# Performance work log

Hardware: AMD Instinct MI355X
Metric: run time of the kernel (lower is better)

## Reference

```python
import jax, jax.numpy as jnp
import numpy as np

B, C, H, W, S = 32, 512, 32, 32, 4
HW = H * W
OUT = HW // S  # conv1/conv2 out channels = 256
EPS = 1e-5


def setup_inputs() -> dict:
    key = jax.random.key(0)
    ks = jax.random.split(key, 8)
    d = {}
    d["x"] = jax.random.normal(ks[0], (B, C, H, W), jnp.float32)
    # conv1 / bn1 (operate on x_flat with 'channels' = h*w)
    d["w1"] = jax.random.normal(ks[1], (OUT, HW), jnp.float32) * 0.02
    d["b1"] = jnp.zeros((OUT,), jnp.float32)
    d["g1"] = jnp.ones((OUT,), jnp.float32)
    d["be1"] = jnp.zeros((OUT,), jnp.float32)
    d["m1"] = jax.random.normal(ks[2], (OUT,), jnp.float32) * 0.01
    d["v1"] = jnp.ones((OUT,), jnp.float32)
    # conv2 / bn2
    d["w2"] = jax.random.normal(ks[3], (OUT, HW), jnp.float32) * 0.02
    d["b2"] = jnp.zeros((OUT,), jnp.float32)
    d["g2"] = jnp.ones((OUT,), jnp.float32)
    d["be2"] = jnp.zeros((OUT,), jnp.float32)
    d["m2"] = jax.random.normal(ks[4], (OUT,), jnp.float32) * 0.01
    d["v2"] = jnp.ones((OUT,), jnp.float32)
    # conv3 / bn3 (1x1 conv on the real channel dim c)
    d["w3"] = jax.random.normal(ks[5], (C, C), jnp.float32) * 0.02
    d["b3"] = jnp.zeros((C,), jnp.float32)
    d["g3"] = jnp.ones((C,), jnp.float32)
    d["be3"] = jnp.zeros((C,), jnp.float32)
    d["m3"] = jax.random.normal(ks[6], (C,), jnp.float32) * 0.01
    d["v3"] = jnp.ones((C,), jnp.float32)
    # conv4: 1x1 conv mapping 1+2c channels -> 1
    d["w4"] = jax.random.normal(ks[7], (1 + 2 * C,), jnp.float32) * 0.02
    d["b4"] = jnp.zeros((), jnp.float32)
    return d


def _bn1d(t, g, be, m, v):
    # t: [b, o, c]; BatchNorm (eval mode) over channel axis 1
    scale = g / jnp.sqrt(v + EPS)
    return (t - m[:, None]) * scale[:, None] + be[:, None]


def reference(x, w1, b1, g1, be1, m1, v1,
              w2, b2, g2, be2, m2, v2,
              w3, b3, g3, be3, m3, v3,
              w4, b4):
    b, c, h, w = x.shape
    # x_flat: [b, h*w, c] -- conv1/conv2 are 1x1 convs over 'channels' = h*w
    xf = x.reshape(b, c, h * w).transpose(0, 2, 1)
    theta = jax.nn.relu(_bn1d(jnp.einsum('oq,bqc->boc', w1, xf) + b1[:, None],
                              g1, be1, m1, v1))  # [b, OUT, c]
    phi = jax.nn.relu(_bn1d(jnp.einsum('oq,bqc->boc', w2, xf) + b2[:, None],
                            g2, be2, m2, v2))    # [b, OUT, c]
    # per-batch conv2d-as-matmul loop collapses to one batched GEMM:
    # affinity[b, i, j] = sum_k phi[b, k, i] * theta[b, k, j]
    aff = jnp.einsum('bki,bkj->bij', phi, theta)  # [b, c, c]
    # x_embed: 1x1 conv + BN + ReLU + global average pool -> [b, c]
    scale3 = g3 / jnp.sqrt(v3 + EPS)
    xe = jnp.einsum('oc,bchw->bohw', w3, x) + b3[:, None, None]
    xe = jax.nn.relu((xe - m3[:, None, None]) * scale3[:, None, None]
                     + be3[:, None, None])
    xe = xe.mean(axis=(2, 3))  # [b, c]
    # conv4 over y = cat([x_embed, affinity_a, affinity_b], dim=1):
    # affinity_a[b,i,0,p] = aff[b,i,p]; affinity_b[b,i,0,p] = aff[b,p,i]
    logits = (w4[0] * xe
              + jnp.einsum('i,bip->bp', w4[1:1 + c], aff)
              + jnp.einsum('i,bpi->bp', w4[1 + c:], aff)
              + b4)
    a = jax.nn.sigmoid(logits)  # [b, c]
    return x * a[:, :, None, None]
```

## Files before the change

kernel.cpp:

```cpp
#include <hip/hip_runtime.h>
#include <math.h>

#define BB   32
#define CC   512
#define HWW  1024
#define OUTC 256
#define EPSV 1e-5f

typedef __attribute__((ext_vector_type(8))) short bfrag;
typedef __attribute__((ext_vector_type(4))) float f32x4;
typedef __attribute__((ext_vector_type(4))) unsigned int u32x4;

__device__ inline unsigned short f2bf(float x){
  unsigned int uu = __float_as_uint(x);
  uu += 0x7fff + ((uu >> 16) & 1);
  return (unsigned short)(uu >> 16);
}
__device__ inline float bf2f(unsigned short h){
  return __uint_as_float(((unsigned int)h) << 16);
}
__device__ inline void packpair(float v0, float v1, unsigned int& hw, unsigned int& lw){
  unsigned short h0 = f2bf(v0), h1 = f2bf(v1);
  unsigned short l0 = f2bf(v0 - bf2f(h0)), l1 = f2bf(v1 - bf2f(h1));
  hw = (unsigned int)h0 | ((unsigned int)h1 << 16);
  lw = (unsigned int)l0 | ((unsigned int)l1 << 16);
}


__global__ __launch_bounds__(256) void prep(
    const float* __restrict__ x,
    const float* __restrict__ w1, const float* __restrict__ w2,
    const float* __restrict__ w3,
    unsigned short* __restrict__ Xhi, unsigned short* __restrict__ Xlo,
    unsigned short* __restrict__ XThi,
    unsigned short* __restrict__ Whi, unsigned short* __restrict__ Wlo,
    unsigned short* __restrict__ W3hi,
    float* __restrict__ accz)
{
  const int tid = threadIdx.x;
  if (blockIdx.z == 32) {
    int worker = (blockIdx.y * 16 + blockIdx.x) * 256 + tid;
    accz[worker] = 0.f;
#pragma unroll
    for (int s = 0; s < 2; ++s) {
      int cid  = worker * 2 + s;
      int tile = cid >> 6, l = cid & 63;
      int o = (tile >> 5) * 16 + (l & 15);
      int k = (tile & 31) * 32 + (l >> 4) * 8;
      const float* src = (o < 256) ? (w1 + (size_t)o * 1024 + k)
                                   : (w2 + (size_t)(o - 256) * 1024 + k);
      u32x4 hv, lv;
#pragma unroll
      for (int j = 0; j < 4; ++j) {
        unsigned int hw, lw;
        packpair(src[2 * j], src[2 * j + 1], hw, lw);
        hv[j] = hw; lv[j] = lw;
      }
      size_t base = (size_t)tile * 512 + (size_t)l * 8;
      *(u32x4*)(Whi + base) = hv;
      *(u32x4*)(Wlo + base) = lv;
    }
    {
      int tile = worker >> 6, l = worker & 63;
      int o = (tile >> 4) * 16 + (l & 15);
      int c = (tile & 15) * 32 + (l >> 4) * 8;
      const float* src = w3 + (size_t)o * 512 + c;
      u32x4 hv;
#pragma unroll
      for (int j = 0; j < 4; ++j) {
        unsigned short h0 = f2bf(src[2 * j]), h1 = f2bf(src[2 * j + 1]);
        hv[j] = (unsigned int)h0 | ((unsigned int)h1 << 16);
      }
      *(u32x4*)(W3hi + (size_t)tile * 512 + (size_t)l * 8) = hv;
    }
    return;
  }
  __shared__ float T[64][65];
  const int b = blockIdx.z, c0 = blockIdx.y * 64, p0 = blockIdx.x * 64;
  const int tr = tid >> 4, tc4 = (tid & 15) * 4;
  const float* xb = x + (size_t)b * 524288;
#pragma unroll
  for (int r = 0; r < 4; ++r) {
    int cl = tr + r * 16;
    float4 v = *(const float4*)(xb + (size_t)(c0 + cl) * 1024 + p0 + tc4);
    T[cl][tc4 + 0] = v.x; T[cl][tc4 + 1] = v.y;
    T[cl][tc4 + 2] = v.z; T[cl][tc4 + 3] = v.w;
  }
  __syncthreads();
#pragma unroll
  for (int s = 0; s < 2; ++s) {
    int cid  = tid + s * 256;
    int tile = cid >> 6, l = cid & 63;
    int tileC = tile >> 1, tileP = tile & 1;
    int cl = tileC * 16 + (l & 15);
    int pl = tileP * 32 + (l >> 4) * 8;
    u32x4 hv, lv;
#pragma unroll
    for (int j = 0; j < 4; ++j) {
      unsigned int hw, lw;
      packpair(T[cl][pl + 2 * j], T[cl][pl + 2 * j + 1], hw, lw);
      hv[j] = hw; lv[j] = lw;
    }
    size_t base = (size_t)b * 524288
                + ((size_t)((c0 + cl) >> 4) * 32 + (size_t)((p0 + pl) >> 5)) * 512
                + (size_t)l * 8;
    *(u32x4*)(Xhi + base) = hv;
    *(u32x4*)(Xlo + base) = lv;
  }
#pragma unroll
  for (int s = 0; s < 2; ++s) {
    int cid  = tid + s * 256;
    int tile = cid >> 6, l = cid & 63;
    int tileP = tile >> 1, tileC = tile & 1;
    int pl = tileP * 16 + (l & 15);
    int cl = tileC * 32 + (l >> 4) * 8;
    u32x4 hv;
#pragma unroll
    for (int j = 0; j < 4; ++j) {
      unsigned short h0 = f2bf(T[cl + 2 * j][pl]);
      unsigned short h1 = f2bf(T[cl + 2 * j + 1][pl]);
      hv[j] = (unsigned int)h0 | ((unsigned int)h1 << 16);
    }
    size_t base = (size_t)b * 524288
                + ((size_t)((p0 + pl) >> 4) * 16 + (size_t)((c0 + cl) >> 5)) * 512
                + (size_t)l * 8;
    *(u32x4*)(XThi + base) = hv;
  }
}

__global__ __launch_bounds__(256, 3) void gemm_fused(
    const unsigned short* __restrict__ Xhi, const unsigned short* __restrict__ Xlo,
    const unsigned short* __restrict__ Whi, const unsigned short* __restrict__ Wlo,
    const unsigned short* __restrict__ W3hi, const unsigned short* __restrict__ XThi,
    const float* __restrict__ b1p, const float* __restrict__ g1p,
    const float* __restrict__ be1p, const float* __restrict__ m1p, const float* __restrict__ v1p,
    const float* __restrict__ b2p, const float* __restrict__ g2p,
    const float* __restrict__ be2p, const float* __restrict__ m2p, const float* __restrict__ v2p,
    const float* __restrict__ b3p, const float* __restrict__ g3p,
    const float* __restrict__ be3p, const float* __restrict__ m3p, const float* __restrict__ v3p,
    const float* __restrict__ w4,
    float* __restrict__ P2, float* __restrict__ u, float* __restrict__ t,
    float* __restrict__ xe_acc)
{
  const int fid  = blockIdx.x;
  const int tid  = threadIdx.x;
  const int wave = tid >> 6, lane = tid & 63;
  const int fr = lane & 15, fq = lane >> 4;

  if (fid < 512) {
    const int xcd = fid & 7;
    const int n0  = ((fid >> 3) & 3) * 128;
    const int bc  = ((fid >> 5) << 3) | xcd;
    const int b   = bc >> 2;
    const int c0  = (bc & 3) * 128;
    const int wm = wave & 1, wn = wave >> 1;

    const bfrag* Ah = (const bfrag*)Xhi + (size_t)b * 65536
                    + (size_t)((c0 >> 4) + wm * 4) * 2048 + lane;
    const bfrag* Al = (const bfrag*)Xlo + (size_t)b * 65536
                    + (size_t)((c0 >> 4) + wm * 4) * 2048 + lane;
    const bfrag* Bh = (const bfrag*)Whi + (size_t)((n0 >> 4) + wn * 4) * 2048 + lane;
    const bfrag* Bl = (const bfrag*)Wlo + (size_t)((n0 >> 4) + wn * 4) * 2048 + lane;

    f32x4 acc[4][4];
    const f32x4 zz = {0.f, 0.f, 0.f, 0.f};
#pragma unroll
    for (int i = 0; i < 4; ++i)
#pragma unroll
      for (int j = 0; j < 4; ++j) acc[i][j] = zz;

#pragma unroll 2
    for (int kq = 0; kq < 32; ++kq) {
      bfrag ah[4], al[4], bh[4], bl[4];
#pragma unroll
      for (int j = 0; j < 4; ++j) {
        bh[j] = Bh[(size_t)j * 2048 + kq * 64];
        bl[j] = Bl[(size_t)j * 2048 + kq * 64];
      }
#pragma unroll
      for (int i = 0; i < 4; ++i) {
        ah[i] = Ah[(size_t)i * 2048 + kq * 64];
        al[i] = Al[(size_t)i * 2048 + kq * 64];
      }
#pragma unroll
      for (int i = 0; i < 4; ++i)
#pragma unroll
        for (int j = 0; j < 4; ++j) {
          acc[i][j] = __builtin_amdgcn_mfma_f32_16x16x32_bf16(ah[i], bh[j], acc[i][j], 0, 0, 0);
          acc[i][j] = __builtin_amdgcn_mfma_f32_16x16x32_bf16(ah[i], bl[j], acc[i][j], 0, 0, 0);
          acc[i][j] = __builtin_amdgcn_mfma_f32_16x16x32_bf16(al[i], bh[j], acc[i][j], 0, 0, 0);
        }
    }

    const float *bias, *gg, *bes, *mm, *vv_; int cof;
    if (n0 < 256) { bias = b1p; gg = g1p; bes = be1p; mm = m1p; vv_ = v1p; cof = 0; }
    else          { bias = b2p; gg = g2p; bes = be2p; mm = m2p; vv_ = v2p; cof = 256; }
    const float* wsel = (n0 < 256) ? (w4 + 513) : (w4 + 1);
    float* dsel = (n0 < 256) ? (t + b * 256) : (u + b * 256);
    const int cobase = (n0 - cof) + wn * 64;
    float wt[4][4];
#pragma unroll
    for (int i = 0; i < 4; ++i)
#pragma unroll
      for (int r = 0; r < 4; ++r)
        wt[i][r] = wsel[c0 + wm * 64 + i * 16 + fq * 4 + r];

#pragma unroll
    for (int j = 0; j < 4; ++j) {
      int co = n0 + wn * 64 + j * 16 + fr;
      int q = co - cof;
      float s  = gg[q] * rsqrtf(vv_[q] + EPSV);
      float sh = (bias[q] - mm[q]) * s + bes[q];
      float psum = 0.f;
#pragma unroll
      for (int i = 0; i < 4; ++i) {
        int crow = c0 + wm * 64 + i * 16 + fq * 4;
        float* dst = P2 + ((size_t)b * 512 + crow) * 512 + co;
#pragma unroll
        for (int r = 0; r < 4; ++r) {
          float val = fmaxf(acc[i][j][r] * s + sh, 0.f);
          dst[(size_t)r * 512] = val;
          psum += wt[i][r] * val;
        }
      }
      psum += __shfl_xor(psum, 16);
      psum += __shfl_xor(psum, 32);
      if (fq == 0) atomicAdd(&dsel[cobase + j * 16 + fr], psum);
    }
  } else {
    const int h  = fid - 512;
    const int n0 = (h & 7) * 128;
    const int m0 = ((h >> 3) & 3) * 128;
    const int b  = h >> 5;
    const int wm = wave & 1, wn = wave >> 1;

    const bfrag* Af = (const bfrag*)W3hi + (size_t)((m0 >> 4) + wm * 4) * 1024 + lane;
    const bfrag* Bf = (const bfrag*)XThi + (size_t)b * 65536
                    + (size_t)((n0 >> 4) + wn * 4) * 1024 + lane;

    f32x4 acc[4][4];
    const f32x4 zz = {0.f, 0.f, 0.f, 0.f};
#pragma unroll
    for (int i = 0; i < 4; ++i)
#pragma unroll
      for (int j = 0; j < 4; ++j) acc[i][j] = zz;

#pragma unroll 2
    for (int kq = 0; kq < 16; ++kq) {
      bfrag af[4], bf4[4];
#pragma unroll
      for (int i = 0; i < 4; ++i)
        af[i] = Af[(size_t)i * 1024 + kq * 64];
#pragma unroll
      for (int j = 0; j < 4; ++j)
        bf4[j] = Bf[(size_t)j * 1024 + kq * 64];
#pragma unroll
      for (int i = 0; i < 4; ++i)
#pragma unroll
        for (int j = 0; j < 4; ++j)
          acc[i][j] = __builtin_amdgcn_mfma_f32_16x16x32_bf16(af[i], bf4[j], acc[i][j], 0, 0, 0);
    }

#pragma unroll
    for (int i = 0; i < 4; ++i) {
#pragma unroll
      for (int r = 0; r < 4; ++r) {
        int o = m0 + wm * 64 + i * 16 + fq * 4 + r;
        float s  = g3p[o] * rsqrtf(v3p[o] + EPSV);
        float sh = (b3p[o] - m3p[o]) * s + be3p[o];
        float v = fmaxf(acc[i][0][r] * s + sh, 0.f) + fmaxf(acc[i][1][r] * s + sh, 0.f)
                + fmaxf(acc[i][2][r] * s + sh, 0.f) + fmaxf(acc[i][3][r] * s + sh, 0.f);
        v += __shfl_xor(v, 1); v += __shfl_xor(v, 2);
        v += __shfl_xor(v, 4); v += __shfl_xor(v, 8);
        if (fr == 0) atomicAdd(&xe_acc[b * 512 + o], v);
      }
    }
  }
}

__global__ __launch_bounds__(256) void k4_gate_out(
    const float* __restrict__ P2, const float* __restrict__ u,
    const float* __restrict__ t, const float* __restrict__ xe_acc,
    const float* __restrict__ w4, const float* __restrict__ b4,
    const float* __restrict__ x, float* __restrict__ out)
{
  __shared__ float us[256], ts[256];
  const int b = blockIdx.x;
  us[threadIdx.x] = u[b * 256 + threadIdx.x];
  ts[threadIdx.x] = t[b * 256 + threadIdx.x];
  __syncthreads();
  const int wave = threadIdx.x >> 6, lane = threadIdx.x & 63;
  const int p = blockIdx.y * 4 + wave;
  const float* row = P2 + ((size_t)b * 512 + p) * 512;
  float4 th = *(const float4*)&row[lane * 4];
  float4 ph = *(const float4*)&row[256 + lane * 4];
  int ki = lane * 4;
  float rs = th.x * us[ki] + th.y * us[ki + 1] + th.z * us[ki + 2] + th.w * us[ki + 3]
           + ph.x * ts[ki] + ph.y * ts[ki + 1] + ph.z * ts[ki + 2] + ph.w * ts[ki + 3];
  rs += __shfl_xor(rs, 1);  rs += __shfl_xor(rs, 2);  rs += __shfl_xor(rs, 4);
  rs += __shfl_xor(rs, 8);  rs += __shfl_xor(rs, 16); rs += __shfl_xor(rs, 32);
  float xe = xe_acc[b * 512 + p] * (1.f / 1024.f);
  float logit = w4[0] * xe + rs + b4[0];
  float a = 1.f / (1.f + expf(-logit));
  const float4* xr = (const float4*)(x + ((size_t)b * 512 + p) * 1024);
  float4* orow = (float4*)(out + ((size_t)b * 512 + p) * 1024);
#pragma unroll
  for (int r2 = 0; r2 < 4; ++r2) {
    float4 xv = xr[lane + r2 * 64];
    float4 ov; ov.x = xv.x * a; ov.y = xv.y * a; ov.z = xv.z * a; ov.w = xv.w * a;
    orow[lane + r2 * 64] = ov;
  }
}

__global__ __launch_bounds__(256) void k1_theta_phi(
    const float* __restrict__ x,
    const float* __restrict__ w1, const float* __restrict__ b1,
    const float* __restrict__ g1, const float* __restrict__ be1,
    const float* __restrict__ m1, const float* __restrict__ v1,
    const float* __restrict__ w2, const float* __restrict__ b2,
    const float* __restrict__ g2, const float* __restrict__ be2,
    const float* __restrict__ m2, const float* __restrict__ v2,
    float* __restrict__ P)
{
  __shared__ __align__(16) float Ws[32][68];
  __shared__ __align__(16) float Xs[32][68];
  const int b  = blockIdx.z;
  const int o0 = blockIdx.y * 64;
  const int c0 = blockIdx.x * 64;
  const int tid = threadIdx.x;
  const int tx = tid & 15, ty = tid >> 4;
  const float* __restrict__ Wbase = (o0 < OUTC) ? (w1 + (size_t)o0 * HWW)
                                                : (w2 + (size_t)(o0 - OUTC) * HWW);
  const float* __restrict__ xb = x + (size_t)b * CC * HWW;
  float acc[4][4] = {{0.f}};
  for (int k0 = 0; k0 < HWW; k0 += 32) {
#pragma unroll
    for (int r = 0; r < 2; ++r) {
      int id  = tid + (r << 8);
      int row = id >> 3;
      int cg  = (id & 7) << 2;
      float4 wv = *(const float4*)(Wbase + (size_t)row * HWW + k0 + cg);
      Ws[cg+0][row] = wv.x; Ws[cg+1][row] = wv.y; Ws[cg+2][row] = wv.z; Ws[cg+3][row] = wv.w;
      float4 xv = *(const float4*)(xb + (size_t)(c0 + row) * HWW + k0 + cg);
      Xs[cg+0][row] = xv.x; Xs[cg+1][row] = xv.y; Xs[cg+2][row] = xv.z; Xs[cg+3][row] = xv.w;
    }
    __syncthreads();
#pragma unroll
    for (int k = 0; k < 32; ++k) {
      float4 av = *(const float4*)&Ws[k][ty * 4];
      float4 bv = *(const float4*)&Xs[k][tx * 4];
      acc[0][0] += av.x*bv.x; acc[0][1] += av.x*bv.y; acc[0][2] += av.x*bv.z; acc[0][3] += av.x*bv.w;
      acc[1][0] += av.y*bv.x; acc[1][1] += av.y*bv.y; acc[1][2] += av.y*bv.z; acc[1][3] += av.y*bv.w;
      acc[2][0] += av.z*bv.x; acc[2][1] += av.z*bv.y; acc[2][2] += av.z*bv.z; acc[2][3] += av.z*bv.w;
      acc[3][0] += av.w*bv.x; acc[3][1] += av.w*bv.y; acc[3][2] += av.w*bv.z; acc[3][3] += av.w*bv.w;
    }
    __syncthreads();
  }
  const float *bias, *g, *be, *m, *v; int ob;
  if (o0 < OUTC) { bias = b1; g = g1; be = be1; m = m1; v = v1; ob = o0; }
  else           { bias = b2; g = g2; be = be2; m = m2; v = v2; ob = o0 - OUTC; }
#pragma unroll
  for (int i = 0; i < 4; ++i) {
    int oi = ob + ty * 4 + i;
    float sc = g[oi] * rsqrtf(v[oi] + EPSV);
    float sh = be[oi] - m[oi] * sc;
    float bb = bias[oi];
    float4 ov;
    ov.x = fmaxf((acc[i][0] + bb) * sc + sh, 0.f);
    ov.y = fmaxf((acc[i][1] + bb) * sc + sh, 0.f);
    ov.z = fmaxf((acc[i][2] + bb) * sc + sh, 0.f);
    ov.w = fmaxf((acc[i][3] + bb) * sc + sh, 0.f);
    int oo = o0 + ty * 4 + i;
    *(float4*)(P + ((size_t)b * 512 + oo) * 512 + c0 + tx * 4) = ov;
  }
}

__global__ __launch_bounds__(256) void k2_xe(
    const float* __restrict__ x, const float* __restrict__ w3,
    const float* __restrict__ b3, const float* __restrict__ g3,
    const float* __restrict__ be3, const float* __restrict__ m3,
    const float* __restrict__ v3, float* __restrict__ xe_acc)
{
  __shared__ __align__(16) float As[32][68];
  __shared__ __align__(16) float Bs[32][68];
  const int b  = blockIdx.z;
  const int o0 = blockIdx.y * 64;
  const int p0 = blockIdx.x * 64;
  const int tid = threadIdx.x;
  const int tx = tid & 15, ty = tid >> 4;
  const float* __restrict__ xb = x + (size_t)b * CC * HWW;
  float acc[4][4] = {{0.f}};
  for (int ck = 0; ck < CC; ck += 32) {
#pragma unroll
    for (int r = 0; r < 2; ++r) {
      int id  = tid + (r << 8);
      int row = id >> 3;
      int cg  = (id & 7) << 2;
      float4 wv = *(const float4*)(w3 + (size_t)(o0 + row) * CC + ck + cg);
      As[cg+0][row] = wv.x; As[cg+1][row] = wv.y; As[cg+2][row] = wv.z; As[cg+3][row] = wv.w;
      int brow = id >> 4;
      int pg   = (id & 15) << 2;
      float4 xv = *(const float4*)(xb + (size_t)(ck + brow) * HWW + p0 + pg);
      *(float4*)&Bs[brow][pg] = xv;
    }
    __syncthreads();
#pragma unroll
    for (int k = 0; k < 32; ++k) {
      float4 av = *(const float4*)&As[k][ty * 4];
      float4 bv = *(const float4*)&Bs[k][tx * 4];
      acc[0][0] += av.x*bv.x; acc[0][1] += av.x*bv.y; acc[0][2] += av.x*bv.z; acc[0][3] += av.x*bv.w;
      acc[1][0] += av.y*bv.x; acc[1][1] += av.y*bv.y; acc[1][2] += av.y*bv.z; acc[1][3] += av.y*bv.w;
      acc[2][0] += av.z*bv.x; acc[2][1] += av.z*bv.y; acc[2][2] += av.z*bv.z; acc[2][3] += av.z*bv.w;
      acc[3][0] += av.w*bv.x; acc[3][1] += av.w*bv.y; acc[3][2] += av.w*bv.z; acc[3][3] += av.w*bv.w;
    }
    __syncthreads();
  }
#pragma unroll
  for (int i = 0; i < 4; ++i) {
    int oo = o0 + ty * 4 + i;
    float sc = g3[oo] * rsqrtf(v3[oo] + EPSV);
    float sh = be3[oo] - m3[oo] * sc;
    float bb = b3[oo];
    float ps = fmaxf((acc[i][0] + bb) * sc + sh, 0.f)
             + fmaxf((acc[i][1] + bb) * sc + sh, 0.f)
             + fmaxf((acc[i][2] + bb) * sc + sh, 0.f)
             + fmaxf((acc[i][3] + bb) * sc + sh, 0.f);
    ps += __shfl_xor(ps, 1);
    ps += __shfl_xor(ps, 2);
    ps += __shfl_xor(ps, 4);
    ps += __shfl_xor(ps, 8);
    if (tx == 0) atomicAdd(&xe_acc[b * CC + oo], ps);
  }
}

__global__ __launch_bounds__(256) void k3_ut(
    const float* __restrict__ P, const float* __restrict__ w4,
    float* __restrict__ u, float* __restrict__ t)
{
  const int b = blockIdx.x;
  const int wv = threadIdx.x >> 6, lane = threadIdx.x & 63;
  const int k = blockIdx.y * 4 + wv;
  const float* __restrict__ w4a = w4 + 1;
  const float* __restrict__ w4b = w4 + 1 + CC;
  const float* __restrict__ throw_ = P + ((size_t)b * 512 + k) * 512;
  const float* __restrict__ phrow  = P + ((size_t)b * 512 + 256 + k) * 512;
  float su = 0.f, st = 0.f;
#pragma unroll
  for (int i = lane; i < CC; i += 64) {
    su += w4a[i] * phrow[i];
    st += w4b[i] * throw_[i];
  }
#pragma unroll
  for (int off = 32; off > 0; off >>= 1) {
    su += __shfl_down(su, off);
    st += __shfl_down(st, off);
  }
  if (lane == 0) { u[b * OUTC + k] = su; t[b * OUTC + k] = st; }
}

__global__ __launch_bounds__(256) void k4_gate(
    const float* __restrict__ P, const float* __restrict__ u,
    const float* __restrict__ t, const float* __restrict__ xe_acc,
    const float* __restrict__ w4, const float* __restrict__ b4,
    float* __restrict__ amul)
{
  __shared__ float us[256], ts[256];
  const int b = blockIdx.x;
  const int p = blockIdx.y * 256 + threadIdx.x;
  us[threadIdx.x] = u[b * OUTC + threadIdx.x];
  ts[threadIdx.x] = t[b * OUTC + threadIdx.x];
  __syncthreads();
  const float* __restrict__ theta = P + (size_t)b * 512 * 512;
  const float* __restrict__ phi   = theta + 256 * 512;
  float r = 0.f, s = 0.f;
#pragma unroll 8
  for (int k = 0; k < OUTC; ++k) {
    r += us[k] * theta[(size_t)k * 512 + p];
    s += ts[k] * phi[(size_t)k * 512 + p];
  }
  float xe = xe_acc[b * CC + p] * (1.0f / 1024.0f);
  float logit = w4[0] * xe + r + s + b4[0];
  amul[b * CC + p] = 1.0f / (1.0f + expf(-logit));
}

__global__ __launch_bounds__(256) void k5_out(
    const float* __restrict__ x, const float* __restrict__ amul,
    float* __restrict__ out)
{
  int i = blockIdx.x * 256 + threadIdx.x;
  float4 xv = ((const float4*)x)[i];
  float a = amul[i >> 8];
  float4 ov; ov.x = xv.x * a; ov.y = xv.y * a; ov.z = xv.z * a; ov.w = xv.w * a;
  ((float4*)out)[i] = ov;
}

extern "C" void kernel_launch(void* const* d_in, const int* in_sizes, int n_in,
                              void* d_out, int out_size, void* d_ws, size_t ws_size,
                              hipStream_t stream)
{
  (void)in_sizes; (void)n_in; (void)out_size;
  const float* x   = (const float*)d_in[0];
  const float* w1  = (const float*)d_in[1];
  const float* b1  = (const float*)d_in[2];
  const float* g1  = (const float*)d_in[3];
  const float* be1 = (const float*)d_in[4];
  const float* m1  = (const float*)d_in[5];
  const float* v1  = (const float*)d_in[6];
  const float* w2  = (const float*)d_in[7];
  const float* b2  = (const float*)d_in[8];
  const float* g2  = (const float*)d_in[9];
  const float* be2 = (const float*)d_in[10];
  const float* m2  = (const float*)d_in[11];
  const float* v2  = (const float*)d_in[12];
  const float* w3  = (const float*)d_in[13];
  const float* b3  = (const float*)d_in[14];
  const float* g3  = (const float*)d_in[15];
  const float* be3 = (const float*)d_in[16];
  const float* m3  = (const float*)d_in[17];
  const float* v3  = (const float*)d_in[18];
  const float* w4  = (const float*)d_in[19];
  const float* b4  = (const float*)d_in[20];
  float* out = (float*)d_out;

  if (ws_size >= 136970240ull) {
    float* P2     = (float*)d_ws;
    float* xe_acc = P2 + 8388608;
    float* u      = P2 + 8404992;
    float* t      = P2 + 8413184;
    unsigned short* Xhi  = (unsigned short*)((char*)d_ws + 33685504);
    unsigned short* Xlo  = Xhi + 16777216;
    unsigned short* XThi = Xlo + 16777216;
    unsigned short* Whi  = XThi + 16777216;
    unsigned short* Wlo  = Whi + 524288;
    unsigned short* W3hi = Wlo + 524288;

    prep<<<dim3(16, 8, 33), 256, 0, stream>>>(x, w1, w2, w3, Xhi, Xlo, XThi,
                                              Whi, Wlo, W3hi, xe_acc);
    gemm_fused<<<dim3(1536), 256, 0, stream>>>(Xhi, Xlo, Whi, Wlo, W3hi, XThi,
        b1, g1, be1, m1, v1, b2, g2, be2, m2, v2, b3, g3, be3, m3, v3,
        w4, P2, u, t, xe_acc);
    k4_gate_out<<<dim3(32, 128), 256, 0, stream>>>(P2, u, t, xe_acc, w4, b4, x, out);
  } else {
    float* P      = (float*)d_ws;
    float* xe_acc = P + (size_t)BB * 512 * 512;
    float* u      = xe_acc + BB * CC;
    float* t      = u + BB * OUTC;
    float* amul   = t + BB * OUTC;

    hipMemsetAsync(xe_acc, 0, (size_t)BB * CC * sizeof(float), stream);

    dim3 blk(256);
    k1_theta_phi<<<dim3(8, 8, BB), blk, 0, stream>>>(x, w1, b1, g1, be1, m1, v1,
                                                     w2, b2, g2, be2, m2, v2, P);
    k2_xe<<<dim3(16, 8, BB), blk, 0, stream>>>(x, w3, b3, g3, be3, m3, v3, xe_acc);
    k3_ut<<<dim3(BB, 64), blk, 0, stream>>>(P, w4, u, t);
    k4_gate<<<dim3(BB, 2), blk, 0, stream>>>(P, u, t, xe_acc, w4, b4, amul);
    k5_out<<<dim3((BB * CC * HWW / 4) / 256), blk, 0, stream>>>(x, amul, out);
  }
}
```

Measured before the change: 269.2 us.

## Stage GEMM operands through double-buffered LDS with async global-to-LDS loads

Both GEMM paths in the fused kernel now stage their A/B fragments through a 64 KB shared-memory double buffer. Each wave issues global_load_lds copies for its own operand slice, and all waves then read the tiles from LDS. Previously every wave loaded its fragments straight from global memory, so the two waves sharing a row or column tile loaded the same data twice. The change removes that duplicate traffic and overlaps the next k-step's loads with the current MFMAs. In exchange it adds two block barriers per iteration and lowers the occupancy hint from 3 to 2 blocks per CU because of the LDS footprint.

New measurement: 257.4 us. 4.4% less time.

```diff
diff --git a/kernel.cpp b/kernel.cpp
--- a/kernel.cpp
+++ b/kernel.cpp
@@ -25,6 +25,11 @@
   hw = (unsigned int)h0 | ((unsigned int)h1 << 16);
   lw = (unsigned int)l0 | ((unsigned int)l1 << 16);
 }
+
+#define ASYNC16(g, l) \
+  __builtin_amdgcn_global_load_lds((const __attribute__((address_space(1))) unsigned int*)(g), \
+                                   (__attribute__((address_space(3))) unsigned int*)(l), 16, 0, 0)
+#define WAITV(N) asm volatile("s_waitcnt vmcnt(" #N ")" ::: "memory")
 
 
 __global__ __launch_bounds__(256) void prep(
@@ -128,7 +133,7 @@
   }
 }
 
-__global__ __launch_bounds__(256, 3) void gemm_fused(
+__global__ __launch_bounds__(256, 2) void gemm_fused(
     const unsigned short* __restrict__ Xhi, const unsigned short* __restrict__ Xlo,
     const unsigned short* __restrict__ Whi, const unsigned short* __restrict__ Wlo,
     const unsigned short* __restrict__ W3hi, const unsigned short* __restrict__ XThi,
@@ -142,6 +147,7 @@
     float* __restrict__ P2, float* __restrict__ u, float* __restrict__ t,
     float* __restrict__ xe_acc)
 {
+  __shared__ unsigned short smem[32768];
   const int fid  = blockIdx.x;
   const int tid  = threadIdx.x;
   const int wave = tid >> 6, lane = tid & 63;
@@ -155,12 +161,13 @@
     const int c0  = (bc & 3) * 128;
     const int wm = wave & 1, wn = wave >> 1;
 
-    const bfrag* Ah = (const bfrag*)Xhi + (size_t)b * 65536
-                    + (size_t)((c0 >> 4) + wm * 4) * 2048 + lane;
-    const bfrag* Al = (const bfrag*)Xlo + (size_t)b * 65536
-                    + (size_t)((c0 >> 4) + wm * 4) * 2048 + lane;
-    const bfrag* Bh = (const bfrag*)Whi + (size_t)((n0 >> 4) + wn * 4) * 2048 + lane;
-    const bfrag* Bl = (const bfrag*)Wlo + (size_t)((n0 >> 4) + wn * 4) * 2048 + lane;
+    const unsigned short* gsrc;
+    int ldst;
+    if (wave == 0)      { gsrc = Xhi + (size_t)b * 524288 + (size_t)(c0 >> 4) * 16384; ldst = 0; }
+    else if (wave == 1) { gsrc = Xlo + (size_t)b * 524288 + (size_t)(c0 >> 4) * 16384; ldst = 4096; }
+    else if (wave == 2) { gsrc = Whi + (size_t)(n0 >> 4) * 16384; ldst = 8192; }
+    else                { gsrc = Wlo + (size_t)(n0 >> 4) * 16384; ldst = 12288; }
+    gsrc += (size_t)lane * 8;
 
     f32x4 acc[4][4];
     const f32x4 zz = {0.f, 0.f, 0.f, 0.f};
@@ -169,18 +176,36 @@
 #pragma unroll
       for (int j = 0; j < 4; ++j) acc[i][j] = zz;
 
-#pragma unroll 2
+#pragma unroll
+    for (int i = 0; i < 8; ++i)
+      ASYNC16(gsrc + (size_t)i * 16384, smem + ldst + i * 512);
+
+    int cur = 0;
     for (int kq = 0; kq < 32; ++kq) {
+      __builtin_amdgcn_sched_barrier(0);
+      if (kq + 1 < 32) {
+        unsigned short* nb = smem + (cur ^ 1) * 16384 + ldst;
+#pragma unroll
+        for (int i = 0; i < 8; ++i)
+          ASYNC16(gsrc + (size_t)i * 16384 + (kq + 1) * 512, nb + i * 512);
+        WAITV(8);
+      } else {
+        WAITV(0);
+      }
+      __builtin_amdgcn_s_barrier();
+      __builtin_amdgcn_sched_barrier(0);
+
+      const unsigned short* bufc = smem + cur * 16384;
       bfrag ah[4], al[4], bh[4], bl[4];
 #pragma unroll
+      for (int i = 0; i < 4; ++i) {
+        ah[i] = *(const bfrag*)&bufc[(wm * 4 + i) * 512 + lane * 8];
+        al[i] = *(const bfrag*)&bufc[4096 + (wm * 4 + i) * 512 + lane * 8];
+      }
+#pragma unroll
       for (int j = 0; j < 4; ++j) {
-        bh[j] = Bh[(size_t)j * 2048 + kq * 64];
-        bl[j] = Bl[(size_t)j * 2048 + kq * 64];
-      }
-#pragma unroll
-      for (int i = 0; i < 4; ++i) {
-        ah[i] = Ah[(size_t)i * 2048 + kq * 64];
-        al[i] = Al[(size_t)i * 2048 + kq * 64];
+        bh[j] = *(const bfrag*)&bufc[8192 + (wn * 4 + j) * 512 + lane * 8];
+        bl[j] = *(const bfrag*)&bufc[12288 + (wn * 4 + j) * 512 + lane * 8];
       }
 #pragma unroll
       for (int i = 0; i < 4; ++i)
@@ -190,7 +215,11 @@
           acc[i][j] = __builtin_amdgcn_mfma_f32_16x16x32_bf16(ah[i], bl[j], acc[i][j], 0, 0, 0);
           acc[i][j] = __builtin_amdgcn_mfma_f32_16x16x32_bf16(al[i], bh[j], acc[i][j], 0, 0, 0);
         }
-    }
+      __builtin_amdgcn_sched_barrier(0);
+      __builtin_amdgcn_s_barrier();
+      cur ^= 1;
+    }
+    __builtin_amdgcn_sched_barrier(0);
 
     const float *bias, *gg, *bes, *mm, *vv_; int cof;
     if (n0 < 256) { bias = b1p; gg = g1p; bes = be1p; mm = m1p; vv_ = v1p; cof = 0; }
@@ -234,9 +263,12 @@
     const int b  = h >> 5;
     const int wm = wave & 1, wn = wave >> 1;
 
-    const bfrag* Af = (const bfrag*)W3hi + (size_t)((m0 >> 4) + wm * 4) * 1024 + lane;
-    const bfrag* Bf = (const bfrag*)XThi + (size_t)b * 65536
-                    + (size_t)((n0 >> 4) + wn * 4) * 1024 + lane;
+    const unsigned short* gsrc;
+    int ldst;
+    if (wave < 2) { gsrc = W3hi + (size_t)((m0 >> 4) + wave * 4) * 8192; ldst = wave * 2048; }
+    else { gsrc = XThi + (size_t)b * 524288 + (size_t)((n0 >> 4) + (wave - 2) * 4) * 8192;
+           ldst = 4096 + (wave - 2) * 2048; }
+    gsrc += (size_t)lane * 8;
 
     f32x4 acc[4][4];
     const f32x4 zz = {0.f, 0.f, 0.f, 0.f};
@@ -245,21 +277,43 @@
 #pragma unroll
       for (int j = 0; j < 4; ++j) acc[i][j] = zz;
 
-#pragma unroll 2
+#pragma unroll
+    for (int i = 0; i < 4; ++i)
+      ASYNC16(gsrc + (size_t)i * 8192, smem + ldst + i * 512);
+
+    int cur = 0;
     for (int kq = 0; kq < 16; ++kq) {
+      __builtin_amdgcn_sched_barrier(0);
+      if (kq + 1 < 16) {
+        unsigned short* nb = smem + (cur ^ 1) * 8192 + ldst;
+#pragma unroll
+        for (int i = 0; i < 4; ++i)
+          ASYNC16(gsrc + (size_t)i * 8192 + (kq + 1) * 512, nb + i * 512);
+        WAITV(4);
+      } else {
+        WAITV(0);
+      }
+      __builtin_amdgcn_s_barrier();
+      __builtin_amdgcn_sched_barrier(0);
+
+      const unsigned short* bufc = smem + cur * 8192;
       bfrag af[4], bf4[4];
 #pragma unroll
       for (int i = 0; i < 4; ++i)
-        af[i] = Af[(size_t)i * 1024 + kq * 64];
+        af[i] = *(const bfrag*)&bufc[(wm * 4 + i) * 512 + lane * 8];
 #pragma unroll
       for (int j = 0; j < 4; ++j)
-        bf4[j] = Bf[(size_t)j * 1024 + kq * 64];
+        bf4[j] = *(const bfrag*)&bufc[4096 + (wn * 4 + j) * 512 + lane * 8];
 #pragma unroll
       for (int i = 0; i < 4; ++i)
 #pragma unroll
         for (int j = 0; j < 4; ++j)
           acc[i][j] = __builtin_amdgcn_mfma_f32_16x16x32_bf16(af[i], bf4[j], acc[i][j], 0, 0, 0);
-    }
+      __builtin_amdgcn_sched_barrier(0);
+      __builtin_amdgcn_s_barrier();
+      cur ^= 1;
+    }
+    __builtin_amdgcn_sched_barrier(0);
 
 #pragma unroll
     for (int i = 0; i < 4; ++i) {
```
